# Optimization experiments

Hardware: AMD Instinct MI355X
Metric: run time of the kernel (lower is better)

The kernel has to match this reference:

```python
import jax, jax.numpy as jnp
import numpy as np
import math

GRID = 256       # grid_size
KMAX = 64        # max_elements_per_cell
RES = 512        # image resolution
SPAN = 4         # max grid cells per axis covered by one triangle bbox
NUM_VIEWS = 16
SCALE = 0.5


def _projection_matrix(x=0.5, n=1.5, f=100.0):
    return np.array([[n / x, 0.0, 0.0, 0.0],
                     [0.0, n / -x, 0.0, 0.0],
                     [0.0, 0.0, -(f + n) / (f - n), -(2.0 * f * n) / (f - n)],
                     [0.0, 0.0, -1.0, 0.0]], dtype=np.float32)


def _view_buffers(num_views, seed):
    rng = np.random.default_rng(seed)
    proj = _projection_matrix()
    mvps, lights = [], []
    for _ in range(num_views):
        u1, u2, u3 = rng.random(3)
        qx = math.sqrt(1.0 - u1) * math.sin(math.tau * u2)
        qy = math.sqrt(1.0 - u1) * math.cos(math.tau * u2)
        qz = math.sqrt(u1) * math.sin(math.tau * u3)
        qw = math.sqrt(u1) * math.cos(math.tau * u3)
        rot = np.array([[1 - 2 * (qy * qy + qz * qz), 2 * (qx * qy - qz * qw), 2 * (qx * qz + qy * qw)],
                        [2 * (qx * qy + qz * qw), 1 - 2 * (qx * qx + qz * qz), 2 * (qy * qz - qx * qw)],
                        [2 * (qx * qz - qy * qw), 2 * (qy * qz + qx * qw), 1 - 2 * (qx * qx + qy * qy)]], dtype=np.float32)
        rmat = np.eye(4, dtype=np.float32); rmat[:3, :3] = rot
        tmat = np.eye(4, dtype=np.float32); tmat[2, 3] = -4.0
        view = tmat @ rmat
        campos = np.linalg.inv(view)[:3, 3]
        light = -campos / (np.linalg.norm(campos) + 1e-8)
        mvps.append(proj @ view)
        lights.append(light.astype(np.float32))
    return np.stack(mvps).astype(np.float32), np.stack(lights).astype(np.float32)


def setup_inputs() -> dict:
    key = jax.random.key(0)
    k1, k2 = jax.random.split(key)
    F = 100_000
    # clustered per-triangle vertices -> small on-screen triangles (mesh-like locality)
    centers = jax.random.uniform(k1, (F, 1, 3), minval=-1.0, maxval=1.0)
    jitter = jax.random.normal(k2, (F, 3, 3)) * 0.02
    u = (centers + jitter).reshape(-1, 3).astype(jnp.float32)          # [3F,3]
    faces = jnp.arange(3 * F, dtype=jnp.int32).reshape(F, 3)
    mvps, light = _view_buffers(NUM_VIEWS, 42)
    return {"u": u,
            "mvps": jnp.asarray(mvps),
            "lightdir": jnp.asarray(light),
            "background_color": jnp.zeros(3, jnp.float32),
            "base_colors": jnp.ones((F, 3), jnp.float32),
            "faces": faces}


def _forward(u, mvps, lightdir, background_color, base_colors, faces):
    # _normalize_vertices
    v = u - u.mean(0, keepdims=True)
    span = jnp.maximum(v.max() - v.min(), 1e-6)
    v = v * (SCALE / span)
    Fn = faces.shape[0]
    # project with active view 0 (v_hom @ mvps[0].T, no perspective divide, as in source)
    v_hom = jnp.concatenate([v, jnp.ones((v.shape[0], 1), v.dtype)], axis=1)
    v_ndc = v_hom @ mvps[0].T                                          # [V,4]
    tris = v_ndc[faces]                                                # [F,3,4]
    wtri = v[faces]                                                    # [F,3,3]
    nrm = jnp.cross(wtri[:, 0] - wtri[:, 1], wtri[:, 2] - wtri[:, 1])
    nrm = nrm / (jnp.linalg.norm(nrm, axis=-1, keepdims=True) + 1e-10)
    z = tris[:, :, 2].mean(1)
    order = jnp.argsort(z)                                             # depth sort (near first)
    st = tris[order]
    sn = nrm[order]
    cp = (st[:, :, :2] + 1.0) * 0.5                                    # [F,3,2] control pts in [0,1]
    shading = jnp.clip(jnp.sum(-lightdir[0] * sn, axis=-1, keepdims=True), 0.0)
    colors = base_colors[order] * shading                              # [F,3]
    # --- grid acceleration structure build (scatter triangles into cells) ---
    lo = jnp.clip(jnp.floor(cp.min(1) * GRID).astype(jnp.int32), 0, GRID - 1)  # [F,2]
    hi = jnp.clip(jnp.floor(cp.max(1) * GRID).astype(jnp.int32), 0, GRID - 1)
    d = jnp.arange(SPAN, dtype=jnp.int32)
    cx = lo[:, 0:1] + d[None, :]                                       # [F,SPAN]
    cy = lo[:, 1:2] + d[None, :]
    valid = (cy[:, :, None] <= hi[:, 1:2, None]) & (cx[:, None, :] <= hi[:, 0:1].reshape(Fn, 1, 1) + 0 * cx[:, None, :])
    valid = (cy[:, :, None] <= hi[:, 1:2, None]) & (cx[:, None, :] <= hi[:, 0:1][:, :, None])
    cell = cy[:, :, None] * GRID + cx[:, None, :]                      # [F,SPAN,SPAN]
    NC = GRID * GRID
    cell = jnp.where(valid, cell, NC).reshape(-1)
    tri = jnp.broadcast_to(jnp.arange(Fn, dtype=jnp.int32)[:, None, None], (Fn, SPAN, SPAN)).reshape(-1)
    # sort (cell, depth-rank): tri ids are already depth-ordered
    keys = cell.astype(jnp.int64) * (Fn + 1) + tri
    ordk = jnp.argsort(keys)
    sc = cell[ordk]
    stri = tri[ordk]
    counts = jax.ops.segment_sum(jnp.ones_like(sc), sc, num_segments=NC + 1)
    starts = jnp.concatenate([jnp.zeros(1, counts.dtype), jnp.cumsum(counts)[:-1]])
    rank = jnp.arange(sc.shape[0], dtype=jnp.int32) - starts[sc].astype(jnp.int32)
    ok = (rank < KMAX) & (sc < NC)
    grid_elems = jnp.full((NC + 1, KMAX), -1, jnp.int32)
    grid_elems = grid_elems.at[jnp.where(ok, sc, NC), jnp.where(ok, rank, 0)].set(jnp.where(ok, stri, -1))
    # --- per-pixel rasterization via grid query ---
    px = (jnp.arange(RES, dtype=jnp.float32) + 0.5) / RES
    uu, vv = jnp.meshgrid(px, px, indexing='xy')
    P = jnp.stack([uu, vv], -1).reshape(-1, 2)                         # [P,2]
    ix = jnp.clip((P[:, 0] * GRID).astype(jnp.int32), 0, GRID - 1)
    iy = jnp.clip((P[:, 1] * GRID).astype(jnp.int32), 0, GRID - 1)
    elems = grid_elems[iy * GRID + ix]                                 # [P,K]
    e = jnp.maximum(elems, 0)
    tpts = cp[e]                                                       # [P,K,3,2]
    a, b, c = tpts[:, :, 0], tpts[:, :, 1], tpts[:, :, 2]
    pp = P[:, None, :]

    def cr(o, q, r):
        return (q[..., 0] - o[..., 0]) * (r[..., 1] - o[..., 1]) - (q[..., 1] - o[..., 1]) * (r[..., 0] - o[..., 0])

    e0 = cr(a, b, pp)
    e1 = cr(b, c, pp)
    e2 = cr(c, a, pp)
    inside = ((e0 >= 0) & (e1 >= 0) & (e2 >= 0)) | ((e0 <= 0) & (e1 <= 0) & (e2 <= 0))
    hit = inside & (elems >= 0)
    first = jnp.argmax(hit, axis=1)                                    # front-most (depth-sorted)
    anyhit = jnp.any(hit, axis=1)
    tid = e[jnp.arange(e.shape[0]), first]
    img = jnp.where(anyhit[:, None], colors[tid], background_color[None, :])
    return img.reshape(RES, RES, 3)


def reference(u, mvps, lightdir, background_color, base_colors, faces):
    return _forward(u, mvps, lightdir, background_color, base_colors, faces)
```

## Files before the change

kernel.cpp:

```cpp
#include <hip/hip_runtime.h>
#include <stdint.h>

#pragma clang fp contract(off)

#define GRIDN 256
#define NC (GRIDN * GRIDN)
#define RESN 512
#define RBLOCKS 256
#define CAP 1024
#define CPB 16
#define NB 32
#define NS 16
#define SBINS 2048


typedef unsigned short bfraw;
typedef unsigned short u16;

__device__ __forceinline__ float bf2f(bfraw h) {
    return __uint_as_float(((uint32_t)h) << 16);
}
__device__ __forceinline__ bfraw f2bf(float f) {
    uint32_t b = __float_as_uint(f);
    return (bfraw)((b + 0x7FFFu + ((b >> 16) & 1u)) >> 16);
}
__device__ __forceinline__ uint32_t fkey(float f) {
    uint32_t b = __float_as_uint(f);
    return (b & 0x80000000u) ? ~b : (b | 0x80000000u);
}

__device__ __forceinline__ void build_pre(const uint32_t* __restrict__ blockSum,
                                          uint32_t* pre) {
    if (threadIdx.x == 0) {
        uint32_t run = 0;
        for (int i = 0; i < 64; i++) { pre[i] = run; run += blockSum[i]; }
        pre[64] = run;
    }
    __syncthreads();
}


__device__ void dev_reduce_partial(const bfraw* __restrict__ u, int nrows, int task,
                                   int t, double* ssum, float* smin, float* smax,
                                   double* __restrict__ psum,
                                   float* __restrict__ pmin,
                                   float* __restrict__ pmax) {
    double s0 = 0.0, s1 = 0.0, s2 = 0.0;
    float mn0 = INFINITY, mn1 = INFINITY, mn2 = INFINITY;
    float mx0 = -INFINITY, mx1 = -INFINITY, mx2 = -INFINITY;
    for (int r = task * 256 + t; r < nrows; r += 256 * RBLOCKS) {
        float a = bf2f(u[3 * r + 0]);
        float b = bf2f(u[3 * r + 1]);
        float c = bf2f(u[3 * r + 2]);
        s0 += (double)a; s1 += (double)b; s2 += (double)c;
        mn0 = fminf(mn0, a); mx0 = fmaxf(mx0, a);
        mn1 = fminf(mn1, b); mx1 = fmaxf(mx1, b);
        mn2 = fminf(mn2, c); mx2 = fmaxf(mx2, c);
    }
    ssum[t * 3 + 0] = s0; ssum[t * 3 + 1] = s1; ssum[t * 3 + 2] = s2;
    smin[t * 3 + 0] = mn0; smin[t * 3 + 1] = mn1; smin[t * 3 + 2] = mn2;
    smax[t * 3 + 0] = mx0; smax[t * 3 + 1] = mx1; smax[t * 3 + 2] = mx2;
    __syncthreads();
    for (int st = 128; st > 0; st >>= 1) {
        if (t < st) {
            for (int c = 0; c < 3; c++) {
                ssum[t * 3 + c] += ssum[(t + st) * 3 + c];
                smin[t * 3 + c] = fminf(smin[t * 3 + c], smin[(t + st) * 3 + c]);
                smax[t * 3 + c] = fmaxf(smax[t * 3 + c], smax[(t + st) * 3 + c]);
            }
        }
        __syncthreads();
    }
    if (t == 0) {
        for (int c = 0; c < 3; c++) {
            psum[task * 3 + c] = ssum[c];
            pmin[task * 3 + c] = smin[c];
            pmax[task * 3 + c] = smax[c];
        }
    }
    __syncthreads();
}

__device__ void dev_reduce_final(const double* __restrict__ psum,
                                 const float* __restrict__ pmin,
                                 const float* __restrict__ pmax,
                                 int nrows, int t,
                                 double* ssum, float* smin, float* smax,
                                 float* __restrict__ cst) {
    for (int c = 0; c < 3; c++) {
        ssum[t * 3 + c] = psum[t * 3 + c];
        smin[t * 3 + c] = pmin[t * 3 + c];
        smax[t * 3 + c] = pmax[t * 3 + c];
    }
    __syncthreads();
    for (int st = 128; st > 0; st >>= 1) {
        if (t < st) {
            for (int c = 0; c < 3; c++) {
                ssum[t * 3 + c] += ssum[(t + st) * 3 + c];
                smin[t * 3 + c] = fminf(smin[t * 3 + c], smin[(t + st) * 3 + c]);
                smax[t * 3 + c] = fmaxf(smax[t * 3 + c], smax[(t + st) * 3 + c]);
            }
        }
        __syncthreads();
    }
    if (t == 0) {
        float fn = (float)nrows;
        float m0 = (float)ssum[0] / fn;
        float m1 = (float)ssum[1] / fn;
        float m2 = (float)ssum[2] / fn;
        float vmax = fmaxf(fmaxf(smax[0] - m0, smax[1] - m1), smax[2] - m2);
        float vmin = fminf(fminf(smin[0] - m0, smin[1] - m1), smin[2] - m2);
        float span = fmaxf(vmax - vmin, 1e-06f);
        float s = 0.5f / span;
        cst[0] = m0; cst[1] = m1; cst[2] = m2; cst[3] = s;
    }
    __syncthreads();
}

__device__ void dev_setup_one(const bfraw* __restrict__ u,
                              const int* __restrict__ faces,
                              const bfraw* __restrict__ mvp,
                              const bfraw* __restrict__ light,
                              const float* __restrict__ cst, int f,
                              float* __restrict__ tcs,
                              uint32_t* __restrict__ tz,
                              uint32_t* __restrict__ tbox) {
    float m0 = cst[0], m1 = cst[1], m2 = cst[2], s = cst[3];
    float M[12];
    for (int i = 0; i < 12; i++) M[i] = bf2f(mvp[i]);

    float vx[3], vy[3], vz[3], cpx[3], cpy[3], zc[3];
    for (int j = 0; j < 3; j++) {
        int idx = faces[3 * f + j];
        float a = bf2f(u[3 * idx + 0]);
        float b = bf2f(u[3 * idx + 1]);
        float c = bf2f(u[3 * idx + 2]);
        float x = (a - m0) * s;
        float y = (b - m1) * s;
        float z = (c - m2) * s;
        vx[j] = x; vy[j] = y; vz[j] = z;
        float cx = fmaf(x, M[0], 0.0f);
        cx = fmaf(y, M[1], cx); cx = fmaf(z, M[2], cx); cx = cx + M[3];
        float cy = fmaf(x, M[4], 0.0f);
        cy = fmaf(y, M[5], cy); cy = fmaf(z, M[6], cy); cy = cy + M[7];
        float cz = fmaf(x, M[8], 0.0f);
        cz = fmaf(y, M[9], cz); cz = fmaf(z, M[10], cz); cz = cz + M[11];
        cpx[j] = (cx + 1.0f) * 0.5f;
        cpy[j] = (cy + 1.0f) * 0.5f;
        zc[j] = cz;
    }
    float zmean = ((zc[0] + zc[1]) + zc[2]) / 3.0f;

    float e1x = vx[0] - vx[1], e1y = vy[0] - vy[1], e1z = vz[0] - vz[1];
    float e2x = vx[2] - vx[1], e2y = vy[2] - vy[1], e2z = vz[2] - vz[1];
    float nx = e1y * e2z - e1z * e2y;
    float ny = e1z * e2x - e1x * e2z;
    float nz = e1x * e2y - e1y * e2x;
    float nn = nx * nx;
    nn = nn + ny * ny;
    nn = nn + nz * nz;
    float d = sqrtf(nn) + 1e-10f;
    float inx = nx / d, iny = ny / d, inz = nz / d;

    float l0 = bf2f(light[0]), l1 = bf2f(light[1]), l2 = bf2f(light[2]);
    float p0 = (-l0) * inx;
    float p1 = (-l1) * iny;
    float p2 = (-l2) * inz;
    float shading = fmaxf((p0 + p1) + p2, 0.0f);

    tcs[f * 8 + 0] = cpx[0]; tcs[f * 8 + 1] = cpy[0];
    tcs[f * 8 + 2] = cpx[1]; tcs[f * 8 + 3] = cpy[1];
    tcs[f * 8 + 4] = cpx[2]; tcs[f * 8 + 5] = cpy[2];
    tcs[f * 8 + 6] = shading;
    tcs[f * 8 + 7] = 0.0f;

    tz[f] = fkey(zmean);

    float mnx = fminf(fminf(cpx[0], cpx[1]), cpx[2]);
    float mny = fminf(fminf(cpy[0], cpy[1]), cpy[2]);
    float mxx = fmaxf(fmaxf(cpx[0], cpx[1]), cpx[2]);
    float mxy = fmaxf(fmaxf(cpy[0], cpy[1]), cpy[2]);
    int lox = (int)floorf(mnx * 256.0f); lox = lox < 0 ? 0 : (lox > 255 ? 255 : lox);
    int loy = (int)floorf(mny * 256.0f); loy = loy < 0 ? 0 : (loy > 255 ? 255 : loy);
    int hix = (int)floorf(mxx * 256.0f); hix = hix < 0 ? 0 : (hix > 255 ? 255 : hix);
    int hiy = (int)floorf(mxy * 256.0f); hiy = hiy < 0 ? 0 : (hiy > 255 ? 255 : hiy);
    int hx = hix < lox + 3 ? hix : lox + 3;
    int hy = hiy < loy + 3 ? hiy : loy + 3;
    tbox[f] = (uint32_t)lox | ((uint32_t)loy << 8) | ((uint32_t)hx << 16) | ((uint32_t)hy << 24);
}

__device__ void dev_count_task(const uint32_t* __restrict__ tbox, int F,
                               u16* __restrict__ blockHist, uint32_t* hist,
                               int task, int t) {
    int b = task >> 4;
    int sl = task & (NS - 1);
    int chunk = (F + NB - 1) / NB;
    int fs = b * chunk;
    int fe = fs + chunk < F ? fs + chunk : F;
    int y0 = sl * 16, y1 = y0 + 15;
    for (int i = t; i < SBINS; i += 256) hist[i] = 0u;
    __syncthreads();
    for (int f = fs + t; f < fe; f += 256) {
        uint32_t bx = tbox[f];
        int lox = bx & 255, loy = (bx >> 8) & 255;
        int hx = (bx >> 16) & 255, hy = bx >> 24;
        int ys = loy > y0 ? loy : y0;
        int ye = hy < y1 ? hy : y1;
        for (int yy = ys; yy <= ye; yy++) {
            for (int xx = lox; xx <= hx; xx++) {
                uint32_t c = (uint32_t)(yy * GRIDN + xx) & 4095u;
                atomicAdd(&hist[c >> 1], 1u << (16u * (c & 1u)));
            }
        }
    }
    __syncthreads();
    uint32_t* dst = (uint32_t*)(blockHist + (size_t)b * NC) + sl * SBINS;
    for (int i = t; i < SBINS; i += 256) dst[i] = hist[i];
    __syncthreads();
}

__device__ void dev_scan_task(u16* __restrict__ blockHist,
                              uint32_t* __restrict__ cellOff,
                              uint32_t* __restrict__ blockSum,
                              uint32_t* sscan, int task, int t) {
    int c0 = task * 1024 + t * 4;
    uint32_t tot[4];
    uint32_t tsum = 0;
    for (int k = 0; k < 4; k++) {
        uint32_t tt = 0;
        for (int b = 0; b < NB; b++) {
            size_t o = (size_t)b * NC + (c0 + k);
            uint32_t v = blockHist[o];
            blockHist[o] = (u16)tt;
            tt += v;
        }
        tot[k] = tt;
        tsum += tt;
    }
    sscan[t] = tsum;
    __syncthreads();
    for (int st = 1; st < 256; st <<= 1) {
        uint32_t a = 0;
        if (t >= st) a = sscan[t - st];
        __syncthreads();
        if (t >= st) sscan[t] += a;
        __syncthreads();
    }
    uint32_t run = sscan[t] - tsum;
    for (int k = 0; k < 4; k++) {
        cellOff[c0 + k] = run;
        run += tot[k];
    }
    if (t == 255) blockSum[task] = sscan[255];
    __syncthreads();
}

__device__ void dev_place_task(const uint32_t* __restrict__ tbox,
                               const u16* __restrict__ blockHist,
                               const uint32_t* __restrict__ cellOff,
                               const uint32_t* pre,
                               uint32_t* __restrict__ pairs, int F,
                               uint32_t* hist, int task, int t) {
    int b = task >> 4;
    int sl = task & (NS - 1);
    int chunk = (F + NB - 1) / NB;
    int fs = b * chunk;
    int fe = fs + chunk < F ? fs + chunk : F;
    int y0 = sl * 16, y1 = y0 + 15;
    uint32_t pcap = (uint32_t)F * 16u;
    for (int i = t; i < SBINS; i += 256) hist[i] = 0u;
    __syncthreads();
    for (int f = fs + t; f < fe; f += 256) {
        uint32_t bx = tbox[f];
        int lox = bx & 255, loy = (bx >> 8) & 255;
        int hx = (bx >> 16) & 255, hy = bx >> 24;
        int ys = loy > y0 ? loy : y0;
        int ye = hy < y1 ? hy : y1;
        for (int yy = ys; yy <= ye; yy++) {
            for (int xx = lox; xx <= hx; xx++) {
                uint32_t cell = (uint32_t)(yy * GRIDN + xx);
                uint32_t c = cell & 4095u;
                uint32_t sh = 16u * (c & 1u);
                uint32_t old = atomicAdd(&hist[c >> 1], 1u << sh);
                uint32_t r = (old >> sh) & 0xFFFFu;
                uint32_t base = cellOff[cell] + pre[cell >> 10];
                uint32_t pos = base + (uint32_t)blockHist[(size_t)b * NC + cell] + r;
                if (pos < pcap) pairs[pos] = (uint32_t)f;
            }
        }
    }
    __syncthreads();
}

__device__ void dev_cellsort_cell(const uint32_t* __restrict__ cellOff,
                                  const uint32_t* pre,
                                  const uint32_t* __restrict__ tz,
                                  uint32_t* __restrict__ pairs, int F,
                                  uint64_t* lkeys, int cell, int t) {
    uint32_t pcap = (uint32_t)F * 16u;
    uint32_t off = cellOff[cell] + pre[cell >> 10];
    uint32_t end = cellOff[cell + 1] + pre[(cell + 1) >> 10];
    if (off > pcap || end > pcap || end < off) return;
    uint32_t n = end - off;
    if (n <= 64u) return;
    uint32_t m = n > CAP ? CAP : n;
    for (uint32_t i = t; i < m; i += 256) {
        uint32_t id = pairs[off + i];
        if (id >= (uint32_t)F) id = 0;
        lkeys[i] = ((uint64_t)tz[id] << 32) | id;
    }
    __syncthreads();
    uint64_t k0 = ~0ull, k1 = ~0ull, k2 = ~0ull, k3 = ~0ull;
    uint32_t i0 = t, i1 = t + 256, i2 = t + 512, i3 = t + 768;
    if (i0 < m) k0 = lkeys[i0];
    if (i1 < m) k1 = lkeys[i1];
    if (i2 < m) k2 = lkeys[i2];
    if (i3 < m) k3 = lkeys[i3];
    uint32_t r0 = 0, r1 = 0, r2 = 0, r3 = 0;
    for (uint32_t j = 0; j < m; j++) {
        uint64_t kj = lkeys[j];
        r0 += (kj < k0) ? 1u : 0u;
        r1 += (kj < k1) ? 1u : 0u;
        r2 += (kj < k2) ? 1u : 0u;
        r3 += (kj < k3) ? 1u : 0u;
    }
    if (i0 < m && r0 < 64u) pairs[off + r0] = (uint32_t)(k0 & 0xFFFFFFFFu);
    if (i1 < m && r1 < 64u) pairs[off + r1] = (uint32_t)(k1 & 0xFFFFFFFFu);
    if (i2 < m && r2 < 64u) pairs[off + r2] = (uint32_t)(k2 & 0xFFFFFFFFu);
    if (i3 < m && r3 < 64u) pairs[off + r3] = (uint32_t)(k3 & 0xFFFFFFFFu);
    __syncthreads();
}

__device__ void dev_raster_pixel(const float* __restrict__ tcs,
                                 const uint32_t* __restrict__ tz,
                                 const uint32_t* __restrict__ cellOff,
                                 const uint32_t* pre,
                                 const uint32_t* __restrict__ pairs,
                                 const bfraw* __restrict__ basec,
                                 const bfraw* __restrict__ bg,
                                 bfraw* __restrict__ out, int F, int p) {
    int col = p & (RESN - 1);
    int row = p >> 9;
    float px = ((float)col + 0.5f) / 512.0f;
    float py = ((float)row + 0.5f) / 512.0f;
    int cell = (row >> 1) * GRIDN + (col >> 1);
    uint32_t pcap = (uint32_t)F * 16u;
    uint32_t off = cellOff[cell] + pre[cell >> 10];
    uint32_t end = cellOff[cell + 1] + pre[(cell + 1) >> 10];
    uint32_t n = 0;
    if (off <= pcap && end <= pcap && end >= off) n = end - off;
    uint32_t m = n > 64u ? 64u : n;
    bool srt = n > 64u;
    uint64_t best = ~0ull;
    uint32_t bestId = 0u;
    float bestSh = 0.0f;
    bool found = false;
    for (uint32_t k = 0; k < m; k++) {
        uint32_t id = pairs[off + k];
        if (id >= (uint32_t)F) continue;
        const float4 A = *(const float4*)(tcs + (size_t)id * 8);
        const float4 B = *(const float4*)(tcs + (size_t)id * 8 + 4);
        float ax = A.x, ay = A.y, bx = A.z, by = A.w, cx = B.x, cy = B.y;
        float e0 = (bx - ax) * (py - ay) - (by - ay) * (px - ax);
        float e1 = (cx - bx) * (py - by) - (cy - by) * (px - bx);
        float e2 = (ax - cx) * (py - cy) - (ay - cy) * (px - cx);
        bool inside = (e0 >= 0.0f && e1 >= 0.0f && e2 >= 0.0f) ||
                      (e0 <= 0.0f && e1 <= 0.0f && e2 <= 0.0f);
        if (inside) {
            if (srt) { bestId = id; bestSh = B.z; found = true; break; }
            uint64_t key = ((uint64_t)tz[id] << 32) | id;
            if (key < best) { best = key; bestId = id; bestSh = B.z; found = true; }
        }
    }
    float r, g, b;
    if (found) {
        r = bf2f(basec[3 * bestId + 0]) * bestSh;
        g = bf2f(basec[3 * bestId + 1]) * bestSh;
        b = bf2f(basec[3 * bestId + 2]) * bestSh;
    } else {
        r = bf2f(bg[0]); g = bf2f(bg[1]); b = bf2f(bg[2]);
    }
    int o = p * 3;
    out[o + 0] = f2bf(r);
    out[o + 1] = f2bf(g);
    out[o + 2] = f2bf(b);
}


__global__ __launch_bounds__(256) void k_reduce1(const bfraw* __restrict__ u, int nrows,
                                                 double* __restrict__ psum,
                                                 float* __restrict__ pmin,
                                                 float* __restrict__ pmax) {
    __shared__ double ssum[768];
    __shared__ float smin[768];
    __shared__ float smax[768];
    dev_reduce_partial(u, nrows, blockIdx.x, threadIdx.x, ssum, smin, smax,
                       psum, pmin, pmax);
}

__global__ __launch_bounds__(256) void k_setup(const bfraw* __restrict__ u,
                                               const int* __restrict__ faces,
                                               const bfraw* __restrict__ mvp,
                                               const bfraw* __restrict__ light,
                                               const double* __restrict__ psum,
                                               const float* __restrict__ pmin,
                                               const float* __restrict__ pmax,
                                               int nrows, int F,
                                               float* __restrict__ tcs,
                                               uint32_t* __restrict__ tz,
                                               uint32_t* __restrict__ tbox) {
    __shared__ double ssum[768];
    __shared__ float smin[768];
    __shared__ float smax[768];
    __shared__ float lcst[4];
    dev_reduce_final(psum, pmin, pmax, nrows, threadIdx.x, ssum, smin, smax, lcst);
    int f = blockIdx.x * 256 + threadIdx.x;
    if (f < F) dev_setup_one(u, faces, mvp, light, lcst, f, tcs, tz, tbox);
}

__global__ __launch_bounds__(256) void k_count(const uint32_t* __restrict__ tbox,
                                               int F, u16* __restrict__ blockHist) {
    __shared__ uint32_t hist[SBINS];
    dev_count_task(tbox, F, blockHist, hist, blockIdx.x, threadIdx.x);
}

__global__ __launch_bounds__(256) void k_scanA(u16* __restrict__ blockHist,
                                               uint32_t* __restrict__ cellOff,
                                               uint32_t* __restrict__ blockSum) {
    __shared__ uint32_t sscan[256];
    dev_scan_task(blockHist, cellOff, blockSum, sscan, blockIdx.x, threadIdx.x);
    if (blockIdx.x == 63 && threadIdx.x == 255) cellOff[NC] = 0u;
}

__global__ __launch_bounds__(256) void k_place(const uint32_t* __restrict__ tbox,
                                               const u16* __restrict__ blockHist,
                                               const uint32_t* __restrict__ cellOff,
                                               const uint32_t* __restrict__ blockSum,
                                               uint32_t* __restrict__ pairs, int F) {
    __shared__ uint32_t hist[SBINS];
    __shared__ uint32_t pre[65];
    build_pre(blockSum, pre);
    dev_place_task(tbox, blockHist, cellOff, pre, pairs, F, hist,
                   blockIdx.x, threadIdx.x);
}

__global__ __launch_bounds__(256) void k_cellsort(const uint32_t* __restrict__ cellOff,
                                                  const uint32_t* __restrict__ blockSum,
                                                  const uint32_t* __restrict__ tz,
                                                  uint32_t* __restrict__ pairs, int F) {
    __shared__ uint64_t lkeys[CAP];
    __shared__ uint32_t pre[65];
    build_pre(blockSum, pre);
    for (int ci = 0; ci < CPB; ci++) {
        int cell = blockIdx.x + ci * (NC / CPB);
        dev_cellsort_cell(cellOff, pre, tz, pairs, F, lkeys, cell, threadIdx.x);
    }
}

__global__ __launch_bounds__(256) void k_raster(const float* __restrict__ tcs,
                                                const uint32_t* __restrict__ tz,
                                                const uint32_t* __restrict__ cellOff,
                                                const uint32_t* __restrict__ blockSum,
                                                const uint32_t* __restrict__ pairs,
                                                const bfraw* __restrict__ basec,
                                                const bfraw* __restrict__ bg,
                                                bfraw* __restrict__ out, int F) {
    __shared__ uint32_t pre[65];
    build_pre(blockSum, pre);
    int p = blockIdx.x * 256 + threadIdx.x;
    dev_raster_pixel(tcs, tz, cellOff, pre, pairs, basec, bg, out, F, p);
}

__global__ __launch_bounds__(256) void k_diag(bfraw* __restrict__ out, float code) {
    out[blockIdx.x * 256 + threadIdx.x] = f2bf(code);
}

extern "C" void kernel_launch(void* const* d_in, const int* in_sizes, int n_in,
                              void* d_out, int out_size, void* d_ws, size_t ws_size,
                              hipStream_t stream) {
    const bfraw* u = (const bfraw*)d_in[0];
    const bfraw* mvps = (const bfraw*)d_in[1];
    const bfraw* light = (const bfraw*)d_in[2];
    const bfraw* bg = (const bfraw*)d_in[3];
    const bfraw* basec = (const bfraw*)d_in[4];
    const int* faces = (const int*)d_in[5];
    int nrows = in_sizes[0] / 3;
    int F = in_sizes[5] / 3;
    bfraw* out = (bfraw*)d_out;

    char* w = (char*)d_ws;
    size_t off = 0;
    auto alloc = [&](size_t bytes) -> void* {
        off = (off + 255) & ~(size_t)255;
        void* p = w + off;
        off += bytes;
        return p;
    };

    double* psum = (double*)alloc((size_t)RBLOCKS * 3 * sizeof(double));
    float* pmin = (float*)alloc((size_t)RBLOCKS * 3 * sizeof(float));
    float* pmax = (float*)alloc((size_t)RBLOCKS * 3 * sizeof(float));
    float* tcs = (float*)alloc((size_t)F * 8 * sizeof(float));
    uint32_t* tz = (uint32_t*)alloc((size_t)F * sizeof(uint32_t));
    uint32_t* tbox = (uint32_t*)alloc((size_t)F * sizeof(uint32_t));
    u16* blockHist = (u16*)alloc((size_t)NB * NC * sizeof(u16));
    uint32_t* cellOff = (uint32_t*)alloc(((size_t)NC + 1) * sizeof(uint32_t));
    uint32_t* blockSum = (uint32_t*)alloc(64 * sizeof(uint32_t));
    uint32_t* pairs = (uint32_t*)alloc((size_t)F * 16 * sizeof(uint32_t));
    size_t needed = off;

    if (ws_size < needed) {
        float code = 20000.0f + (float)(ws_size >> 20);
        k_diag<<<(RESN * RESN * 3) / 256, 256, 0, stream>>>(out, code);
        return;
    }

    k_reduce1<<<RBLOCKS, 256, 0, stream>>>(u, nrows, psum, pmin, pmax);
    k_setup<<<(F + 255) / 256, 256, 0, stream>>>(u, faces, mvps, light,
                                                 psum, pmin, pmax, nrows, F,
                                                 tcs, tz, tbox);
    k_count<<<NB * NS, 256, 0, stream>>>(tbox, F, blockHist);
    k_scanA<<<64, 256, 0, stream>>>(blockHist, cellOff, blockSum);
    k_place<<<NB * NS, 256, 0, stream>>>(tbox, blockHist, cellOff, blockSum,
                                         pairs, F);
    k_cellsort<<<NC / CPB, 256, 0, stream>>>(cellOff, blockSum, tz, pairs, F);
    k_raster<<<(RESN * RESN) / 256, 256, 0, stream>>>(tcs, tz, cellOff, blockSum,
                                                      pairs, basec, bg, out, F);
}
```

Baseline: 160.4 us.

## Rasterize per grid cell with wave-wide triangle tests and parallelize scans

The raster kernel now gives each 64-lane wave one grid cell. Each lane tests one of the cell's up-to-64 triangles against all four pixels of the cell, and a shuffle min-reduction on (depth, id) keys picks the front-most hit. Before, every pixel looped serially over its cell's list. The per-block prefix built by build_pre now uses a wavefront shuffle scan instead of a single-thread loop. k_scanA switches to 1024-thread blocks with one cell per thread, loading all 32 histogram entries before scanning. The wave-level raster removes serial per-pixel loops and duplicate triangle loads, at the cost of shuffle reductions over 64-bit keys and mostly idle lanes when cells are sparse.

```diff
diff --git a/kernel.cpp b/kernel.cpp
--- a/kernel.cpp
+++ b/kernel.cpp
@@ -29,12 +29,18 @@
     return (b & 0x80000000u) ? ~b : (b | 0x80000000u);
 }
 
-__device__ __forceinline__ void build_pre(const uint32_t* __restrict__ blockSum,
-                                          uint32_t* pre) {
-    if (threadIdx.x == 0) {
-        uint32_t run = 0;
-        for (int i = 0; i < 64; i++) { pre[i] = run; run += blockSum[i]; }
-        pre[64] = run;
+__device__ __forceinline__ void build_pre64(const uint32_t* __restrict__ blockSum,
+                                            uint32_t* pre) {
+    int t = threadIdx.x;
+    if (t < 64) {
+        uint32_t v = blockSum[t];
+        uint32_t s = v;
+        for (int d = 1; d < 64; d <<= 1) {
+            uint32_t o = __shfl_up(s, d, 64);
+            if (t >= d) s += o;
+        }
+        pre[t] = s - v;
+        if (t == 63) pre[64] = s;
     }
     __syncthreads();
 }
@@ -219,42 +225,6 @@
     __syncthreads();
 }
 
-__device__ void dev_scan_task(u16* __restrict__ blockHist,
-                              uint32_t* __restrict__ cellOff,
-                              uint32_t* __restrict__ blockSum,
-                              uint32_t* sscan, int task, int t) {
-    int c0 = task * 1024 + t * 4;
-    uint32_t tot[4];
-    uint32_t tsum = 0;
-    for (int k = 0; k < 4; k++) {
-        uint32_t tt = 0;
-        for (int b = 0; b < NB; b++) {
-            size_t o = (size_t)b * NC + (c0 + k);
-            uint32_t v = blockHist[o];
-            blockHist[o] = (u16)tt;
-            tt += v;
-        }
-        tot[k] = tt;
-        tsum += tt;
-    }
-    sscan[t] = tsum;
-    __syncthreads();
-    for (int st = 1; st < 256; st <<= 1) {
-        uint32_t a = 0;
-        if (t >= st) a = sscan[t - st];
-        __syncthreads();
-        if (t >= st) sscan[t] += a;
-        __syncthreads();
-    }
-    uint32_t run = sscan[t] - tsum;
-    for (int k = 0; k < 4; k++) {
-        cellOff[c0 + k] = run;
-        run += tot[k];
-    }
-    if (t == 255) blockSum[task] = sscan[255];
-    __syncthreads();
-}
-
 __device__ void dev_place_task(const uint32_t* __restrict__ tbox,
                                const u16* __restrict__ blockHist,
                                const uint32_t* __restrict__ cellOff,
@@ -329,61 +299,6 @@
     if (i2 < m && r2 < 64u) pairs[off + r2] = (uint32_t)(k2 & 0xFFFFFFFFu);
     if (i3 < m && r3 < 64u) pairs[off + r3] = (uint32_t)(k3 & 0xFFFFFFFFu);
     __syncthreads();
-}
-
-__device__ void dev_raster_pixel(const float* __restrict__ tcs,
-                                 const uint32_t* __restrict__ tz,
-                                 const uint32_t* __restrict__ cellOff,
-                                 const uint32_t* pre,
-                                 const uint32_t* __restrict__ pairs,
-                                 const bfraw* __restrict__ basec,
-                                 const bfraw* __restrict__ bg,
-                                 bfraw* __restrict__ out, int F, int p) {
-    int col = p & (RESN - 1);
-    int row = p >> 9;
-    float px = ((float)col + 0.5f) / 512.0f;
-    float py = ((float)row + 0.5f) / 512.0f;
-    int cell = (row >> 1) * GRIDN + (col >> 1);
-    uint32_t pcap = (uint32_t)F * 16u;
-    uint32_t off = cellOff[cell] + pre[cell >> 10];
-    uint32_t end = cellOff[cell + 1] + pre[(cell + 1) >> 10];
-    uint32_t n = 0;
-    if (off <= pcap && end <= pcap && end >= off) n = end - off;
-    uint32_t m = n > 64u ? 64u : n;
-    bool srt = n > 64u;
-    uint64_t best = ~0ull;
-    uint32_t bestId = 0u;
-    float bestSh = 0.0f;
-    bool found = false;
-    for (uint32_t k = 0; k < m; k++) {
-        uint32_t id = pairs[off + k];
-        if (id >= (uint32_t)F) continue;
-        const float4 A = *(const float4*)(tcs + (size_t)id * 8);
-        const float4 B = *(const float4*)(tcs + (size_t)id * 8 + 4);
-        float ax = A.x, ay = A.y, bx = A.z, by = A.w, cx = B.x, cy = B.y;
-        float e0 = (bx - ax) * (py - ay) - (by - ay) * (px - ax);
-        float e1 = (cx - bx) * (py - by) - (cy - by) * (px - bx);
-        float e2 = (ax - cx) * (py - cy) - (ay - cy) * (px - cx);
-        bool inside = (e0 >= 0.0f && e1 >= 0.0f && e2 >= 0.0f) ||
-                      (e0 <= 0.0f && e1 <= 0.0f && e2 <= 0.0f);
-        if (inside) {
-            if (srt) { bestId = id; bestSh = B.z; found = true; break; }
-            uint64_t key = ((uint64_t)tz[id] << 32) | id;
-            if (key < best) { best = key; bestId = id; bestSh = B.z; found = true; }
-        }
-    }
-    float r, g, b;
-    if (found) {
-        r = bf2f(basec[3 * bestId + 0]) * bestSh;
-        g = bf2f(basec[3 * bestId + 1]) * bestSh;
-        b = bf2f(basec[3 * bestId + 2]) * bestSh;
-    } else {
-        r = bf2f(bg[0]); g = bf2f(bg[1]); b = bf2f(bg[2]);
-    }
-    int o = p * 3;
-    out[o + 0] = f2bf(r);
-    out[o + 1] = f2bf(g);
-    out[o + 2] = f2bf(b);
 }
 
 
@@ -424,12 +339,34 @@
     dev_count_task(tbox, F, blockHist, hist, blockIdx.x, threadIdx.x);
 }
 
-__global__ __launch_bounds__(256) void k_scanA(u16* __restrict__ blockHist,
-                                               uint32_t* __restrict__ cellOff,
-                                               uint32_t* __restrict__ blockSum) {
-    __shared__ uint32_t sscan[256];
-    dev_scan_task(blockHist, cellOff, blockSum, sscan, blockIdx.x, threadIdx.x);
-    if (blockIdx.x == 63 && threadIdx.x == 255) cellOff[NC] = 0u;
+__global__ __launch_bounds__(1024) void k_scanA(u16* __restrict__ blockHist,
+                                                uint32_t* __restrict__ cellOff,
+                                                uint32_t* __restrict__ blockSum) {
+    __shared__ uint32_t sc[1024];
+    int B = blockIdx.x, t = threadIdx.x;
+    int c = B * 1024 + t;
+    uint32_t v[NB];
+#pragma unroll
+    for (int b = 0; b < NB; b++) v[b] = blockHist[(size_t)b * NC + c];
+    uint32_t tot = 0;
+#pragma unroll
+    for (int b = 0; b < NB; b++) {
+        uint32_t x = v[b];
+        blockHist[(size_t)b * NC + c] = (u16)tot;
+        tot += x;
+    }
+    sc[t] = tot;
+    __syncthreads();
+    for (int st = 1; st < 1024; st <<= 1) {
+        uint32_t a = 0;
+        if (t >= st) a = sc[t - st];
+        __syncthreads();
+        if (t >= st) sc[t] += a;
+        __syncthreads();
+    }
+    cellOff[c] = sc[t] - tot;
+    if (t == 1023) blockSum[B] = sc[1023];
+    if (B == 63 && t == 1023) cellOff[NC] = 0u;
 }
 
 __global__ __launch_bounds__(256) void k_place(const uint32_t* __restrict__ tbox,
@@ -439,7 +376,7 @@
                                                uint32_t* __restrict__ pairs, int F) {
     __shared__ uint32_t hist[SBINS];
     __shared__ uint32_t pre[65];
-    build_pre(blockSum, pre);
+    build_pre64(blockSum, pre);
     dev_place_task(tbox, blockHist, cellOff, pre, pairs, F, hist,
                    blockIdx.x, threadIdx.x);
 }
@@ -450,7 +387,7 @@
                                                   uint32_t* __restrict__ pairs, int F) {
     __shared__ uint64_t lkeys[CAP];
     __shared__ uint32_t pre[65];
-    build_pre(blockSum, pre);
+    build_pre64(blockSum, pre);
     for (int ci = 0; ci < CPB; ci++) {
         int cell = blockIdx.x + ci * (NC / CPB);
         dev_cellsort_cell(cellOff, pre, tz, pairs, F, lkeys, cell, threadIdx.x);
@@ -466,9 +403,74 @@
                                                 const bfraw* __restrict__ bg,
                                                 bfraw* __restrict__ out, int F) {
     __shared__ uint32_t pre[65];
-    build_pre(blockSum, pre);
-    int p = blockIdx.x * 256 + threadIdx.x;
-    dev_raster_pixel(tcs, tz, cellOff, pre, pairs, basec, bg, out, F, p);
+    build_pre64(blockSum, pre);
+    int wave = threadIdx.x >> 6;
+    int lane = threadIdx.x & 63;
+    int cell = blockIdx.x * 4 + wave;
+    int cy = cell >> 8, cx = cell & 255;
+    uint32_t pcap = (uint32_t)F * 16u;
+    uint32_t off = cellOff[cell] + pre[cell >> 10];
+    uint32_t end = cellOff[cell + 1] + pre[(cell + 1) >> 10];
+    uint32_t n = 0;
+    if (off <= pcap && end <= pcap && end >= off) n = end - off;
+    uint32_t m = n > 64u ? 64u : n;
+
+    uint64_t kk0 = ~0ull, kk1 = ~0ull, kk2 = ~0ull, kk3 = ~0ull;
+    if (lane < (int)m) {
+        uint32_t id = pairs[off + lane];
+        if (id < (uint32_t)F) {
+            const float4 A = *(const float4*)(tcs + (size_t)id * 8);
+            const float4 B = *(const float4*)(tcs + (size_t)id * 8 + 4);
+            float ax = A.x, ay = A.y, bx = A.z, by = A.w, cxx = B.x, cyy = B.y;
+            uint64_t key = ((uint64_t)tz[id] << 32) | id;
+#pragma unroll
+            for (int i = 0; i < 4; i++) {
+                int col = cx * 2 + (i & 1);
+                int row = cy * 2 + (i >> 1);
+                float px = ((float)col + 0.5f) / 512.0f;
+                float py = ((float)row + 0.5f) / 512.0f;
+                float e0 = (bx - ax) * (py - ay) - (by - ay) * (px - ax);
+                float e1 = (cxx - bx) * (py - by) - (cyy - by) * (px - bx);
+                float e2 = (ax - cxx) * (py - cyy) - (ay - cyy) * (px - cxx);
+                bool inside = (e0 >= 0.0f && e1 >= 0.0f && e2 >= 0.0f) ||
+                              (e0 <= 0.0f && e1 <= 0.0f && e2 <= 0.0f);
+                uint64_t kv = inside ? key : ~0ull;
+                if (i == 0) kk0 = kv;
+                else if (i == 1) kk1 = kv;
+                else if (i == 2) kk2 = kv;
+                else kk3 = kv;
+            }
+        }
+    }
+    for (int d = 1; d < 64; d <<= 1) {
+        uint64_t o0 = __shfl_xor((unsigned long long)kk0, d, 64);
+        uint64_t o1 = __shfl_xor((unsigned long long)kk1, d, 64);
+        uint64_t o2 = __shfl_xor((unsigned long long)kk2, d, 64);
+        uint64_t o3 = __shfl_xor((unsigned long long)kk3, d, 64);
+        kk0 = o0 < kk0 ? o0 : kk0;
+        kk1 = o1 < kk1 ? o1 : kk1;
+        kk2 = o2 < kk2 ? o2 : kk2;
+        kk3 = o3 < kk3 ? o3 : kk3;
+    }
+    if (lane < 4) {
+        uint64_t best = lane == 0 ? kk0 : (lane == 1 ? kk1 : (lane == 2 ? kk2 : kk3));
+        int col = cx * 2 + (lane & 1);
+        int row = cy * 2 + (lane >> 1);
+        float r, g, b;
+        if (best != ~0ull) {
+            uint32_t id = (uint32_t)(best & 0xFFFFFFFFu);
+            float sh = tcs[(size_t)id * 8 + 6];
+            r = bf2f(basec[3 * id + 0]) * sh;
+            g = bf2f(basec[3 * id + 1]) * sh;
+            b = bf2f(basec[3 * id + 2]) * sh;
+        } else {
+            r = bf2f(bg[0]); g = bf2f(bg[1]); b = bf2f(bg[2]);
+        }
+        int o = (row * RESN + col) * 3;
+        out[o + 0] = f2bf(r);
+        out[o + 1] = f2bf(g);
+        out[o + 2] = f2bf(b);
+    }
 }
 
 __global__ __launch_bounds__(256) void k_diag(bfraw* __restrict__ out, float code) {
@@ -520,10 +522,10 @@
                                                  psum, pmin, pmax, nrows, F,
                                                  tcs, tz, tbox);
     k_count<<<NB * NS, 256, 0, stream>>>(tbox, F, blockHist);
-    k_scanA<<<64, 256, 0, stream>>>(blockHist, cellOff, blockSum);
+    k_scanA<<<64, 1024, 0, stream>>>(blockHist, cellOff, blockSum);
     k_place<<<NB * NS, 256, 0, stream>>>(tbox, blockHist, cellOff, blockSum,
                                          pairs, F);
     k_cellsort<<<NC / CPB, 256, 0, stream>>>(cellOff, blockSum, tz, pairs, F);
-    k_raster<<<(RESN * RESN) / 256, 256, 0, stream>>>(tcs, tz, cellOff, blockSum,
-                                                      pairs, basec, bg, out, F);
-}
+    k_raster<<<NC / 4, 256, 0, stream>>>(tcs, tz, cellOff, blockSum,
+                                         pairs, basec, bg, out, F);
+}
```

New measurement: 166.7 us. +4.0%, slower.
